# Kernel tuning notes

Measured on AMD Instinct MI355X. Metric: run time of the kernel, lower is better.

The kernel has to match this reference:

```python
import jax, jax.numpy as jnp
import numpy as np

NUM_HEADS = 16
D_MODEL = 1024
D_K = D_MODEL // NUM_HEADS
THETA = 10000.0
SEQ_LEN = 2048
BATCH = 2


def _rope(x, token_positions):
    # x: [B, H, S, d_k]; token_positions: [S] int
    d_k = x.shape[-1]
    inv_freq = THETA ** (-jnp.arange(0, d_k, 2, dtype=jnp.float32) / d_k)  # [d_k/2]
    ang = token_positions.astype(jnp.float32)[:, None] * inv_freq[None, :]  # [S, d_k/2]
    cos, sin = jnp.cos(ang), jnp.sin(ang)
    x_even = x[..., ::2]
    x_odd = x[..., 1::2]
    rot_even = x_even * cos - x_odd * sin
    rot_odd = x_even * sin + x_odd * cos
    return jnp.stack([rot_even, rot_odd], axis=-1).reshape(x.shape)


def setup_inputs() -> dict:
    key = jax.random.key(0)
    kx, kq, kk, kv, ko = jax.random.split(key, 5)
    sigma = float(np.sqrt(2.0 / (D_MODEL + D_MODEL)))
    x = jax.random.normal(kx, (BATCH, SEQ_LEN, D_MODEL), dtype=jnp.float32)
    Wq = jax.random.truncated_normal(kq, -3.0, 3.0, (D_MODEL, D_MODEL), jnp.float32) * sigma
    Wk = jax.random.truncated_normal(kk, -3.0, 3.0, (D_MODEL, D_MODEL), jnp.float32) * sigma
    Wv = jax.random.truncated_normal(kv, -3.0, 3.0, (D_MODEL, D_MODEL), jnp.float32) * sigma
    Wo = jax.random.truncated_normal(ko, -3.0, 3.0, (D_MODEL, D_MODEL), jnp.float32) * sigma
    token_positions = jnp.arange(SEQ_LEN, dtype=jnp.int32)
    return {"x": x, "Wq": Wq, "Wk": Wk, "Wv": Wv, "Wo": Wo, "token_positions": token_positions}


def reference(x, Wq, Wk, Wv, Wo, token_positions):
    bs, seq_len, _ = x.shape
    # Linear stores W as [out, in]: out = einsum('...i,oi->...o')
    def proj(W):
        h = jnp.einsum('bsi,oi->bso', x, W)
        return h.reshape(bs, seq_len, NUM_HEADS, D_K).transpose(0, 2, 1, 3)  # [B,H,S,d_k]
    Q = _rope(proj(Wq), token_positions)
    K = _rope(proj(Wk), token_positions)
    V = proj(Wv)
    scores = jnp.einsum('bhqd,bhkd->bhqk', Q, K) / jnp.sqrt(jnp.float32(D_K))
    causal = jnp.tril(jnp.ones((seq_len, seq_len), dtype=bool))
    scores = jnp.where(causal[None, None], scores, -jnp.inf)
    probs = jax.nn.softmax(scores, axis=-1)
    attn = jnp.einsum('bhqk,bhkd->bhqd', probs, V)
    attn = attn.transpose(0, 2, 1, 3).reshape(bs, seq_len, NUM_HEADS * D_K)
    return jnp.einsum('bsi,oi->bso', attn, Wo)
```

## Files before the change

kernel.cpp:

```cpp
#include <hip/hip_runtime.h>
#include <math.h>

#define SEQ  2048
#define DM   1024
#define NH   16
#define DK   64
#define MTOT 4096
#define BATCH 2

typedef __attribute__((ext_vector_type(8))) short bf16x8;
typedef __attribute__((ext_vector_type(4))) float f32x4;

#define CSC 0.18033688011112042f
#define FMAX 12.0f

__device__ __forceinline__ ushort f2bf(float f) {
    unsigned u = __builtin_bit_cast(unsigned, f);
    u += 0x7FFFu + ((u >> 16) & 1u);
    return (ushort)(u >> 16);
}

__device__ __forceinline__ void async_ld16(const void* g, void* l) {
    __builtin_amdgcn_global_load_lds(
        (const __attribute__((address_space(1))) void*)g,
        (__attribute__((address_space(3))) void*)l, 16, 0, 0);
}


__global__ __launch_bounds__(256) void convert_kernel(
    const float* __restrict__ X, const float* __restrict__ Wq,
    const float* __restrict__ Wk, const float* __restrict__ Wv,
    const float* __restrict__ Wo, const int* __restrict__ pos,
    ushort* __restrict__ Xb, ushort* __restrict__ Wqkvb,
    ushort* __restrict__ Wob, float2* __restrict__ rtab)
{
    const int y = blockIdx.y;
    if (y == 5) {
        int i = blockIdx.x * 256 + threadIdx.x;
        if (i < SEQ * 32) {
            int s = i >> 5, j = i & 31;
            float freq = exp2f(-(float)(2 * j) * (13.287712379549449f / 64.0f));
            float ang = (float)pos[s] * freq;
            float sn, cs;
            sincosf(ang, &sn, &cs);
            rtab[i] = make_float2(cs, sn);
        }
        return;
    }
    const float* src; ushort* dst; int n;
    if (y == 0)      { src = X;  dst = Xb;                 n = MTOT * DM; }
    else if (y == 1) { src = Wq; dst = Wqkvb;              n = DM * DM; }
    else if (y == 2) { src = Wk; dst = Wqkvb + DM * DM;    n = DM * DM; }
    else if (y == 3) { src = Wv; dst = Wqkvb + 2 * DM * DM; n = DM * DM; }
    else             { src = Wo; dst = Wob;                n = DM * DM; }
    for (int i = (blockIdx.x * 256 + threadIdx.x) * 4; i < n; i += gridDim.x * 256 * 4) {
        float4 v = *(const float4*)(src + i);
        ushort4 o = { f2bf(v.x), f2bf(v.y), f2bf(v.z), f2bf(v.w) };
        *(ushort4*)(dst + i) = o;
    }
}

template <int MODE>
__global__ __launch_bounds__(256, 3) void gemm_mfma(
    const ushort* __restrict__ Agl, const ushort* __restrict__ Bgl,
    const float2* __restrict__ rtab, ushort* __restrict__ O0,
    ushort* __restrict__ O1, ushort* __restrict__ O2,
    float* __restrict__ Fout)
{
    constexpr int BM = (MODE == 0) ? 128 : 64;
    constexpr int BN = 128;
    constexpr int BK = 32;
    constexpr int WM = (MODE == 0) ? 64 : 32;
    constexpr int MT = WM / 16;
    constexpr int NINST = (BM + BN) / 16;
    constexpr int PW = NINST / 4;

    __shared__ __align__(16) ushort S[(BM + BN) * BK];

    const int t    = threadIdx.x;
    const int lane = t & 63;
    const int w    = t >> 6;
    const int wm   = w >> 1, wn = w & 1;
    const int l16  = lane & 15, quad = lane >> 4;
    const int lrow = lane >> 2;
    const int lseg = (lane & 3) * 8;

    const int bn = blockIdx.x, bm = blockIdx.y;
    const int m0 = bm * BM, n0 = bn * BN;

    f32x4 acc[MT][4];
#pragma unroll
    for (int mt = 0; mt < MT; ++mt)
#pragma unroll
        for (int nt = 0; nt < 4; ++nt) acc[mt][nt] = (f32x4){0.f, 0.f, 0.f, 0.f};

    for (int kt = 0; kt < DM / BK; ++kt) {
        __syncthreads();
#pragma unroll
        for (int i = 0; i < PW; ++i) {
            const int rbase = (w * PW + i) * 16;
            const ushort* g;
            if (rbase < BM)
                g = Agl + (size_t)(m0 + rbase + lrow) * DM + kt * BK + lseg;
            else
                g = Bgl + (size_t)(n0 + rbase - BM + lrow) * DM + kt * BK + lseg;
            async_ld16(g, &S[rbase * BK]);
        }
        __syncthreads();

        bf16x8 af[MT], bfr[4];
#pragma unroll
        for (int mt = 0; mt < MT; ++mt)
            af[mt] = *(const bf16x8*)&S[(wm * WM + mt * 16 + l16) * BK + quad * 8];
#pragma unroll
        for (int nt = 0; nt < 4; ++nt)
            bfr[nt] = *(const bf16x8*)&S[(BM + wn * 64 + nt * 16 + l16) * BK + quad * 8];
#pragma unroll
        for (int mt = 0; mt < MT; ++mt)
#pragma unroll
            for (int nt = 0; nt < 4; ++nt)
                acc[mt][nt] = __builtin_amdgcn_mfma_f32_16x16x32_bf16(
                    af[mt], bfr[nt], acc[mt][nt], 0, 0, 0);
    }

    if (MODE == 1) {
#pragma unroll
        for (int mt = 0; mt < MT; ++mt)
#pragma unroll
            for (int r = 0; r < 4; ++r) {
                const int m = m0 + wm * WM + mt * 16 + quad * 4 + r;
#pragma unroll
                for (int nt = 0; nt < 4; ++nt) {
                    const int n = n0 + wn * 64 + nt * 16 + l16;
                    Fout[(size_t)m * DM + n] = acc[mt][nt][r];
                }
            }
    } else {
        const int matb = n0 >> 10;
        if (matb < 2) {
            ushort* img = matb ? O1 : O0;
            const int hh = ((n0 & 1023) + wn * 64) >> 6;
            int dloc[4];
#pragma unroll
            for (int nt = 0; nt < 4; ++nt) dloc[nt] = nt * 16 + l16;
#pragma unroll
            for (int mt = 0; mt < MT; ++mt)
#pragma unroll
                for (int r = 0; r < 4; ++r) {
                    const int m = m0 + wm * WM + mt * 16 + quad * 4 + r;
                    const int bb = m >> 11;
                    const int s = m & 2047;
                    const size_t base =
                        ((size_t)(bb * NH + hh) * 32 + (s >> 6)) * 4096 + (s & 63) * 64;
                    const int swz = s & 7;
#pragma unroll
                    for (int nt = 0; nt < 4; ++nt) {
                        const float v = acc[mt][nt][r];
                        const float vp = __shfl_xor(v, 1);
                        const float2 cs = rtab[s * 32 + (dloc[nt] >> 1)];
                        float res = (dloc[nt] & 1) ? (vp * cs.y + v * cs.x)
                                                   : (v * cs.x - vp * cs.y);
                        if (matb == 0) res *= CSC;
                        const int d = dloc[nt];
                        img[base + (((d >> 3) ^ swz) << 3) + (d & 7)] = f2bf(res);
                    }
                }
        } else {
#pragma unroll
            for (int mt = 0; mt < MT; ++mt)
#pragma unroll
                for (int r = 0; r < 4; ++r) {
                    const int m = m0 + wm * WM + mt * 16 + quad * 4 + r;
                    const int bb = m >> 11;
                    const int s = m & 2047;
#pragma unroll
                    for (int nt = 0; nt < 4; ++nt) {
                        const int dgl = (n0 & 1023) + wn * 64 + nt * 16 + l16;
                        const int hh = dgl >> 6, dd = dgl & 63;
                        const size_t off =
                            ((size_t)(bb * NH + hh) * 32 + (s >> 6)) * 4096 + dd * 64 +
                            ((((s & 63) >> 3) ^ (dd & 7)) << 3) + (s & 7);
                        O2[off] = f2bf(acc[mt][nt][r]);
                    }
                }
        }
    }
}

__global__ __launch_bounds__(256, 2) void attn_mfma(
    const ushort* __restrict__ Qimg, const ushort* __restrict__ Kimg,
    const ushort* __restrict__ Vimg, ushort* __restrict__ Ob)
{
    const int t    = threadIdx.x;
    const int lane = t & 63;
    const int w    = t >> 6;
    const int l16  = lane & 15;
    const int quad = lane >> 4;
    const int swz  = l16 & 7;

    const int id = blockIdx.x;
    const int h  = id & 15;
    const int z  = id >> 4;
    const int b  = z & 1;
    const int p  = z >> 1;
    const int qtB = 31 - p;

    const size_t bh = ((size_t)(b * NH + h)) * 32;
    const ushort* Kh = Kimg + bh * 4096;
    const ushort* Vh = Vimg + bh * 4096;

    __shared__ __align__(16) ushort Ks[2][4096];
    __shared__ __align__(16) ushort Vs[2][4096];
    __shared__ __align__(16) ushort Ps[4096];

#define STAGE_KV(tile, buf)                                                  \
    do {                                                                     \
        const ushort* Kt_ = Kh + (size_t)(tile) * 4096;                      \
        const ushort* Vt_ = Vh + (size_t)(tile) * 4096;                      \
        _Pragma("unroll") for (int i_ = 0; i_ < 2; ++i_) {                   \
            async_ld16(Kt_ + i_ * 2048 + w * 512 + lane * 8,                 \
                       &Ks[buf][i_ * 2048 + w * 512]);                       \
            async_ld16(Vt_ + i_ * 2048 + w * 512 + lane * 8,                 \
                       &Vs[buf][i_ * 2048 + w * 512]);                       \
        }                                                                    \
    } while (0)

    const int qr = w * 16 + l16;

    bf16x8 bQ0, bQ1;
    {
        const ushort* Qt = Qimg + (bh + p) * 4096;
        bQ0 = *(const bf16x8*)(Qt + qr * 64 + ((quad ^ swz) << 3));
        bQ1 = *(const bf16x8*)(Qt + qr * 64 + (((4 + quad) ^ swz) << 3));
    }

    STAGE_KV(0, 0);

    f32x4 Oacc[4];
    float l_i = 0.f;
#pragma unroll
    for (int d = 0; d < 4; ++d) Oacc[d] = (f32x4){0.f, 0.f, 0.f, 0.f};

    int qt = p;

    auto writeO = [&](int qtw) {
        float lf = l_i;
        lf += __shfl_xor(lf, 16);
        lf += __shfl_xor(lf, 32);
#pragma unroll
        for (int r = 0; r < 4; ++r) {
            const float lr = __shfl(lf, (lane & 48) | (quad * 4 + r));
            const float inv = 1.0f / lr;
            const int q_abs = qtw * 64 + w * 16 + quad * 4 + r;
            ushort* dst = Ob + (size_t)(b * SEQ + q_abs) * DM + h * DK + l16;
#pragma unroll
            for (int dblk = 0; dblk < 4; ++dblk)
                dst[dblk * 16] = f2bf(Oacc[dblk][r] * inv);
        }
    };

    for (int it = 0; it <= 32; ++it) {
        const int cur = it & 1;
        const int kt = (it <= p) ? it : it - (p + 1);
        __syncthreads();

        if (it < 32) {
            const int itn = it + 1;
            const int ktn = (itn <= p) ? itn : itn - (p + 1);
            STAGE_KV(ktn, cur ^ 1);
        }

        bf16x8 aK[4][2];
#pragma unroll
        for (int ki = 0; ki < 4; ++ki)
#pragma unroll
            for (int ds = 0; ds < 2; ++ds)
                aK[ki][ds] = *(const bf16x8*)
                    &Ks[cur][(ki * 16 + l16) * 64 + (((ds * 4 + quad) ^ swz) << 3)];
        bf16x8 bV[2][4];
#pragma unroll
        for (int s2 = 0; s2 < 2; ++s2)
#pragma unroll
            for (int dblk = 0; dblk < 4; ++dblk)
                bV[s2][dblk] = *(const bf16x8*)
                    &Vs[cur][(dblk * 16 + l16) * 64 + (((s2 * 4 + quad) ^ swz) << 3)];

        f32x4 Sc[4];
#pragma unroll
        for (int ki = 0; ki < 4; ++ki) {
            Sc[ki] = (f32x4){0.f, 0.f, 0.f, 0.f};
            Sc[ki] = __builtin_amdgcn_mfma_f32_16x16x32_bf16(aK[ki][0], bQ0, Sc[ki], 0, 0, 0);
            Sc[ki] = __builtin_amdgcn_mfma_f32_16x16x32_bf16(aK[ki][1], bQ1, Sc[ki], 0, 0, 0);
        }

        const bool diag = (kt == qt);
        const int qa = w * 16 + l16;
        const int ka = quad * 4;
        const int prow = qr * 64;
        const int phalf = (quad & 1) * 4;
#pragma unroll
        for (int ki = 0; ki < 4; ++ki) {
            float pe[4];
#pragma unroll
            for (int r = 0; r < 4; ++r) {
                const bool masked = diag && (ka + ki * 16 + r > qa);
                pe[r] = masked ? 0.f
                               : __builtin_amdgcn_exp2f(Sc[ki][r] - FMAX);
                l_i += pe[r];
            }
            uint2 pk;
            pk.x = __builtin_amdgcn_perm(__builtin_bit_cast(unsigned, pe[1]),
                                         __builtin_bit_cast(unsigned, pe[0]),
                                         0x07060302u);
            pk.y = __builtin_amdgcn_perm(__builtin_bit_cast(unsigned, pe[3]),
                                         __builtin_bit_cast(unsigned, pe[2]),
                                         0x07060302u);
            const int seg = ki * 2 + (quad >> 1);
            *(uint2*)&Ps[prow + (((seg ^ swz) << 3) + phalf)] = pk;
        }

#pragma unroll
        for (int s2 = 0; s2 < 2; ++s2) {
            bf16x8 aP = *(const bf16x8*)&Ps[prow + (((s2 * 4 + quad) ^ swz) << 3)];
#pragma unroll
            for (int dblk = 0; dblk < 4; ++dblk)
                Oacc[dblk] = __builtin_amdgcn_mfma_f32_16x16x32_bf16(
                    aP, bV[s2][dblk], Oacc[dblk], 0, 0, 0);
        }

        if (it == p) {
            writeO(p);
            l_i = 0.f;
#pragma unroll
            for (int d = 0; d < 4; ++d) Oacc[d] = (f32x4){0.f, 0.f, 0.f, 0.f};
            qt = qtB;
            const ushort* Qt = Qimg + (bh + qtB) * 4096;
            bQ0 = *(const bf16x8*)(Qt + qr * 64 + ((quad ^ swz) << 3));
            bQ1 = *(const bf16x8*)(Qt + qr * 64 + (((4 + quad) ^ swz) << 3));
        }
    }

    writeO(qtB);
#undef STAGE_KV
}

extern "C" void kernel_launch(void* const* d_in, const int* in_sizes, int n_in,
                              void* d_out, int out_size, void* d_ws, size_t ws_size,
                              hipStream_t stream)
{
    const float* x  = (const float*)d_in[0];
    const float* Wq = (const float*)d_in[1];
    const float* Wk = (const float*)d_in[2];
    const float* Wv = (const float*)d_in[3];
    const float* Wo = (const float*)d_in[4];
    const int* pos  = (const int*)d_in[5];
    float* out = (float*)d_out;

    ushort* Xb    = (ushort*)d_ws;
    ushort* Wqkvb = Xb + (size_t)MTOT * DM;
    ushort* Wob   = Wqkvb + (size_t)3 * DM * DM;
    float2* rtab  = (float2*)(Wob + (size_t)DM * DM);
    ushort* Qimg  = (ushort*)(rtab + SEQ * 32);
    ushort* Kimg  = Qimg + (size_t)MTOT * DM;
    ushort* Vimg  = Kimg + (size_t)MTOT * DM;
    ushort* attnb = Vimg + (size_t)MTOT * DM;

    convert_kernel<<<dim3(1024, 6), dim3(256), 0, stream>>>(
        x, Wq, Wk, Wv, Wo, pos, Xb, Wqkvb, Wob, rtab);
    gemm_mfma<0><<<dim3(24, 32), dim3(256), 0, stream>>>(
        Xb, Wqkvb, rtab, Qimg, Kimg, Vimg, nullptr);
    attn_mfma<<<dim3(512), dim3(256), 0, stream>>>(Qimg, Kimg, Vimg, attnb);
    gemm_mfma<1><<<dim3(8, 64), dim3(256), 0, stream>>>(
        attnb, Wob, nullptr, nullptr, nullptr, nullptr, out);
}
```

Baseline: 173.9 us.

## Double GEMM K-tile to 64 with XOR-swizzled LDS layout

Raises the GEMM K tile from 32 to 64, which halves the number of barrier-separated load/compute iterations. Each row is staged as eight 16-byte chunks, and chunk positions are XOR-swizzled by row so the per-lane fragment reads avoid LDS bank conflicts. The inner compute now runs two k-substeps per tile. This doubles the LDS footprint per block, which may reduce occupancy under launch_bounds(256,3).

```diff
diff --git a/kernel.cpp b/kernel.cpp
--- a/kernel.cpp
+++ b/kernel.cpp
@@ -69,21 +69,22 @@
 {
     constexpr int BM = (MODE == 0) ? 128 : 64;
     constexpr int BN = 128;
-    constexpr int BK = 32;
+    constexpr int BK = 64;
     constexpr int WM = (MODE == 0) ? 64 : 32;
     constexpr int MT = WM / 16;
-    constexpr int NINST = (BM + BN) / 16;
+    constexpr int ROWS = BM + BN;
+    constexpr int NINST = ROWS / 8;
     constexpr int PW = NINST / 4;
 
-    __shared__ __align__(16) ushort S[(BM + BN) * BK];
+    __shared__ __align__(16) ushort S[ROWS * BK];
 
     const int t    = threadIdx.x;
     const int lane = t & 63;
     const int w    = t >> 6;
     const int wm   = w >> 1, wn = w & 1;
     const int l16  = lane & 15, quad = lane >> 4;
-    const int lrow = lane >> 2;
-    const int lseg = (lane & 3) * 8;
+    const int lrow8  = lane >> 3;
+    const int lchunk = lane & 7;
 
     const int bn = blockIdx.x, bm = blockIdx.y;
     const int m0 = bm * BM, n0 = bn * BN;
@@ -98,29 +99,38 @@
         __syncthreads();
 #pragma unroll
         for (int i = 0; i < PW; ++i) {
-            const int rbase = (w * PW + i) * 16;
+            const int rbase = (w * PW + i) * 8;
+            const int row = rbase + lrow8;
+            const int sc = lchunk ^ (row & 7);
             const ushort* g;
             if (rbase < BM)
-                g = Agl + (size_t)(m0 + rbase + lrow) * DM + kt * BK + lseg;
+                g = Agl + (size_t)(m0 + row) * DM + kt * BK + sc * 8;
             else
-                g = Bgl + (size_t)(n0 + rbase - BM + lrow) * DM + kt * BK + lseg;
+                g = Bgl + (size_t)(n0 + row - BM) * DM + kt * BK + sc * 8;
             async_ld16(g, &S[rbase * BK]);
         }
         __syncthreads();
 
-        bf16x8 af[MT], bfr[4];
-#pragma unroll
-        for (int mt = 0; mt < MT; ++mt)
-            af[mt] = *(const bf16x8*)&S[(wm * WM + mt * 16 + l16) * BK + quad * 8];
-#pragma unroll
-        for (int nt = 0; nt < 4; ++nt)
-            bfr[nt] = *(const bf16x8*)&S[(BM + wn * 64 + nt * 16 + l16) * BK + quad * 8];
-#pragma unroll
-        for (int mt = 0; mt < MT; ++mt)
-#pragma unroll
-            for (int nt = 0; nt < 4; ++nt)
-                acc[mt][nt] = __builtin_amdgcn_mfma_f32_16x16x32_bf16(
-                    af[mt], bfr[nt], acc[mt][nt], 0, 0, 0);
+#pragma unroll
+        for (int ks = 0; ks < 2; ++ks) {
+            bf16x8 af[MT], bfr[4];
+#pragma unroll
+            for (int mt = 0; mt < MT; ++mt) {
+                const int r = wm * WM + mt * 16 + l16;
+                af[mt] = *(const bf16x8*)&S[r * BK + (((ks * 4 + quad) ^ (r & 7)) << 3)];
+            }
+#pragma unroll
+            for (int nt = 0; nt < 4; ++nt) {
+                const int r = BM + wn * 64 + nt * 16 + l16;
+                bfr[nt] = *(const bf16x8*)&S[r * BK + (((ks * 4 + quad) ^ (r & 7)) << 3)];
+            }
+#pragma unroll
+            for (int mt = 0; mt < MT; ++mt)
+#pragma unroll
+                for (int nt = 0; nt < 4; ++nt)
+                    acc[mt][nt] = __builtin_amdgcn_mfma_f32_16x16x32_bf16(
+                        af[mt], bfr[nt], acc[mt][nt], 0, 0, 0);
+        }
     }
 
     if (MODE == 1) {
```

Result: faster. 169.9 us (-2.3%).
